# Performance work log

Hardware: AMD Instinct MI355X
Metric: run time of the kernel (lower is better)

The kernel has to match this reference:

```python
import jax, jax.numpy as jnp
import numpy as np

B, S, D, H = 4, 2048, 1024, 16
HD = D // H


def setup_inputs() -> dict:
    key = jax.random.key(0)
    ks = jax.random.split(key, 12)
    s = 1.0 / np.sqrt(D)
    return {
        "query": jax.random.normal(ks[0], (B, S, D), jnp.float32),
        "key_": jax.random.normal(ks[1], (B, S, D), jnp.float32),
        "value": jax.random.normal(ks[2], (B, S, D), jnp.float32),
        "mask": jnp.ones((1, 1, S, S), dtype=bool),
        "Wq": jax.random.normal(ks[3], (D, D), jnp.float32) * s,
        "bq": jnp.zeros((D,), jnp.float32),
        "Wk": jax.random.normal(ks[4], (D, D), jnp.float32) * s,
        "bk": jnp.zeros((D,), jnp.float32),
        "Wv": jax.random.normal(ks[5], (D, D), jnp.float32) * s,
        "bv": jnp.zeros((D,), jnp.float32),
        "Wo": jax.random.normal(ks[6], (D, D), jnp.float32) * s,
        "bo": jnp.zeros((D,), jnp.float32),
    }


def reference(query, key_, value, mask, Wq, bq, Wk, bk, Wv, bv, Wo, bo):
    # Linear projections (torch Linear: x @ W^T + b; here W stored as (in, out))
    Q = query @ Wq + bq   # [B,S,D]
    K = key_ @ Wk + bk
    V = value @ Wv + bv
    # split heads -> [B,H,S,HD]
    Q = Q.reshape(B, S, H, HD).transpose(0, 2, 1, 3)
    K = K.reshape(B, S, H, HD).transpose(0, 2, 1, 3)
    V = V.reshape(B, S, H, HD).transpose(0, 2, 1, 3)
    scores = jnp.einsum("bhqd,bhkd->bhqk", Q, K) / jnp.sqrt(jnp.float32(HD))
    scores = jnp.where(mask, scores, jnp.float32(-jnp.inf))
    attn = jax.nn.softmax(scores, axis=-1)          # [B,H,S,S]
    ctx = jnp.einsum("bhqk,bhkd->bhqd", attn, V)    # dropout = identity (eval)
    ctx = ctx.transpose(0, 2, 1, 3).reshape(B, S, D)
    out = ctx @ Wo + bo
    return out, attn
```

## Files before the change

### kernel.cpp

```cpp
#include <hip/hip_runtime.h>

typedef __attribute__((ext_vector_type(4))) unsigned short u16x4;
typedef __attribute__((ext_vector_type(8))) short short8;
typedef __attribute__((ext_vector_type(4))) short short4b;
typedef __attribute__((ext_vector_type(4))) float f32x4;

__device__ inline unsigned short f2bf(float f) {
    union { float f; unsigned int i; } v; v.f = f;
    unsigned int r = v.i + 0x7fffu + ((v.i >> 16) & 1u);
    return (unsigned short)(r >> 16);
}

#define MFMA_PV(a, b, c) __builtin_amdgcn_mfma_f32_16x16x16bf16_1k((a), (b), (c), 0, 0, 0)
#define MFMA32(a, b, c) __builtin_amdgcn_mfma_f32_16x16x32_bf16((a), (b), (c), 0, 0, 0)

#define SEXP(s) exp2f((s) * 0.18033688011112042f)

__device__ inline void gload_lds16(const unsigned short* g, unsigned short* l) {
    __builtin_amdgcn_global_load_lds(
        (const __attribute__((address_space(1))) void*)g,
        (__attribute__((address_space(3))) void*)l,
        16, 0, 0);
}

__global__ __launch_bounds__(256) void prep(const float* __restrict__ q,
                                            const float* __restrict__ k,
                                            const float* __restrict__ v,
                                            const float* __restrict__ W0,
                                            const float* __restrict__ W1,
                                            const float* __restrict__ W2,
                                            const float* __restrict__ W3,
                                            unsigned short* __restrict__ Xq,
                                            unsigned short* __restrict__ Xk,
                                            unsigned short* __restrict__ Xv,
                                            unsigned short* __restrict__ O0,
                                            unsigned short* __restrict__ O1,
                                            unsigned short* __restrict__ O2,
                                            unsigned short* __restrict__ O3) {
    __shared__ unsigned short tile[32][33];
    int bid = blockIdx.x;
    if (bid < 24576) {
        const float* in = (bid < 8192) ? q : (bid < 16384) ? k : v;
        unsigned short* out = (bid < 8192) ? Xq : (bid < 16384) ? Xk : Xv;
        int i = (bid & 8191) * 256 + threadIdx.x;
        float4 vv = ((const float4*)in)[i];
        u16x4 o = { f2bf(vv.x), f2bf(vv.y), f2bf(vv.z), f2bf(vv.w) };
        ((u16x4*)out)[i] = o;
    } else {
        int rem = bid - 24576;
        int z = rem >> 10, idx = rem & 1023;
        const float* in = (z == 0) ? W0 : (z == 1) ? W1 : (z == 2) ? W2 : W3;
        unsigned short* out = (z == 0) ? O0 : (z == 1) ? O1 : (z == 2) ? O2 : O3;
        int c0 = (idx & 31) * 32, r0 = (idx >> 5) * 32;
        int x = threadIdx.x & 31, y = threadIdx.x >> 5;
#pragma unroll
        for (int i = 0; i < 4; i++)
            tile[y + i * 8][x] = f2bf(in[(size_t)(r0 + y + i * 8) * 1024 + c0 + x]);
        __syncthreads();
#pragma unroll
        for (int i = 0; i < 4; i++)
            out[(size_t)(c0 + y + i * 8) * 1024 + r0 + x] = tile[x][y + i * 8];
    }
}

__device__ __forceinline__ void gemm_core(const unsigned short* __restrict__ X,
                                          const unsigned short* __restrict__ Wt,
                                          unsigned short* As, unsigned short* Bs,
                                          int m0, int n0, int K, f32x4 acc[4][4]) {
    const int t = threadIdx.x;
    const int l = t & 63, w = t >> 6;
    const int lg = l >> 4, ln = l & 15;
    const int wm = (w >> 1) * 64, wn = (w & 1) * 64;

    int sr[4], sc[4];
#pragma unroll
    for (int i = 0; i < 4; i++) {
        int pos = i * 2048 + t * 8;
        sr[i] = pos >> 6;
        int c8 = (pos >> 3) & 7;
        sc[i] = (c8 ^ (sr[i] & 7)) * 8;
    }

    for (int k0 = 0; k0 < K; k0 += 64) {
#pragma unroll
        for (int i = 0; i < 4; i++)
            gload_lds16(&X[(size_t)(m0 + sr[i]) * K + k0 + sc[i]], &As[i * 2048 + w * 512]);
#pragma unroll
        for (int i = 0; i < 4; i++)
            gload_lds16(&Wt[(size_t)(n0 + sr[i]) * K + k0 + sc[i]], &Bs[i * 2048 + w * 512]);
        __syncthreads();
#pragma unroll
        for (int kk = 0; kk < 2; kk++) {
            short8 af[4], bfr[4];
#pragma unroll
            for (int i = 0; i < 4; i++) {
                int sl = (((kk << 2) | lg) ^ (ln & 7)) * 8;
                af[i]  = *(const short8*)&As[(wm + i * 16 + ln) * 64 + sl];
                bfr[i] = *(const short8*)&Bs[(wn + i * 16 + ln) * 64 + sl];
            }
#pragma unroll
            for (int i = 0; i < 4; i++)
#pragma unroll
                for (int j = 0; j < 4; j++)
                    acc[i][j] = MFMA32(af[i], bfr[j], acc[i][j]);
        }
        __syncthreads();
    }
}

__global__ __launch_bounds__(256) void gemm_qk(const unsigned short* __restrict__ Xq,
                                               const unsigned short* __restrict__ Xk,
                                               const unsigned short* __restrict__ WqT,
                                               const unsigned short* __restrict__ WkT,
                                               const float* __restrict__ bq,
                                               const float* __restrict__ bk,
                                               unsigned short* __restrict__ Qp,
                                               unsigned short* __restrict__ Kt) {
    __shared__ unsigned short As[8192];
    __shared__ unsigned short Bs[8192];
    const int z = blockIdx.z;
    const unsigned short* X = z ? Xk : Xq;
    const unsigned short* Wt = z ? WkT : WqT;
    const float* bias = z ? bk : bq;
    const int t = threadIdx.x, l = t & 63, w = t >> 6;
    const int lg = l >> 4, ln = l & 15;
    const int wm = (w >> 1) * 64, wn = (w & 1) * 64;
    const int m0 = blockIdx.y * 128, n0 = blockIdx.x * 128;

    const f32x4 zero = {0.f, 0.f, 0.f, 0.f};
    f32x4 acc[4][4];
#pragma unroll
    for (int i = 0; i < 4; i++)
#pragma unroll
        for (int j = 0; j < 4; j++) acc[i][j] = zero;

    gemm_core(X, Wt, As, Bs, m0, n0, 1024, acc);

#pragma unroll
    for (int j = 0; j < 4; j++) {
        int gn = n0 + wn + j * 16 + ln;
        float bvv = bias[gn];
#pragma unroll
        for (int i = 0; i < 4; i++) {
            int gm = m0 + wm + i * 16 + 4 * lg;
#pragma unroll
            for (int jj = 0; jj < 4; jj++) {
                float val = acc[i][j][jj] + bvv;
                int m = gm + jj, n = gn;
                if (z) {
                    int b = m >> 11, s = m & 2047;
                    int itk = s >> 5, r = s & 31;
                    int h = n >> 6, dl = n & 63;
                    int cst = (dl >> 3) ^ (r & 7);
                    size_t off = (size_t)(b * 16 + h) * 131072 +
                                 (size_t)itk * 2048 + r * 64 + cst * 8 + (dl & 7);
                    Kt[off] = f2bf(val);
                } else {
                    Qp[(size_t)m * 1024 + n] = f2bf(val);
                }
            }
        }
    }
}

__global__ __launch_bounds__(256) void gemmv_pass1(const unsigned short* __restrict__ Xv,
                                                   const unsigned short* __restrict__ WvT,
                                                   const float* __restrict__ bv,
                                                   unsigned short* __restrict__ Vt,
                                                   const unsigned short* __restrict__ Qp,
                                                   const unsigned short* __restrict__ Kt,
                                                   float* __restrict__ se_buf) {
    const int S = 2048, Dm = 1024;
    __shared__ unsigned short smem[16384];

    int bid = blockIdx.x;
    int t = threadIdx.x, l = t & 63, w = t >> 6;
    int lg = l >> 4, ln = l & 15;

    if (bid >= 1024) {
        int g = bid - 1024;
        const int wm = (w >> 1) * 64, wn = (w & 1) * 64;
        const int m0 = (g >> 3) * 128, n0 = (g & 7) * 128;
        const f32x4 zero = {0.f, 0.f, 0.f, 0.f};
        f32x4 acc[4][4];
#pragma unroll
        for (int i = 0; i < 4; i++)
#pragma unroll
            for (int j = 0; j < 4; j++) acc[i][j] = zero;

        gemm_core(Xv, WvT, smem, smem + 8192, m0, n0, 1024, acc);

#pragma unroll
        for (int j = 0; j < 4; j++) {
            int gn = n0 + wn + j * 16 + ln;
            float bvv = bv[gn];
#pragma unroll
            for (int i = 0; i < 4; i++) {
                int gm = m0 + wm + i * 16 + 4 * lg;
#pragma unroll
                for (int jj = 0; jj < 4; jj++) {
                    float val = acc[i][j][jj] + bvv;
                    int m = gm + jj, n = gn;
                    int b = m >> 11, s = m & 2047;
                    int h = n >> 6, dl = n & 63;
                    size_t off = (size_t)(b * 16 + h) * 131072 +
                                 (size_t)(s >> 5) * 2048 + ((s >> 4) & 1) * 1024 +
                                 dl * 16 + (s & 15);
                    Vt[off] = f2bf(val);
                }
            }
        }
        return;
    }

    int wid = (bid & 7) * 128 + (bid >> 3);
    int qt = wid & 15, bh = wid >> 4;
    int b = bh >> 4, h = bh & 15;
    int qbase = qt * 128 + w * 16;

    const unsigned short* Qr0 = Qp + (size_t)(b * S + qbase + ln) * Dm + h * 64;
    const unsigned short* Qr1 = Qr0 + (size_t)64 * Dm;
    short8 q00 = *(const short8*)&Qr0[8 * lg];
    short8 q01 = *(const short8*)&Qr0[32 + 8 * lg];
    short8 q10 = *(const short8*)&Qr1[8 * lg];
    short8 q11 = *(const short8*)&Qr1[32 + 8 * lg];

    const unsigned short* Kb = Kt + (size_t)bh * 131072;
    const int c0x = (lg ^ (ln & 7)) * 8;
    const int c1x = ((4 + lg) ^ (ln & 7)) * 8;
    const int gb[4] = { ln * 64, 1024 + ln * 64, 2048 + ln * 64, 3072 + ln * 64 };

#define STAGE_K64(it, buf) do { \
    gload_lds16(Kb + (size_t)(it) * 4096 + t * 8, &smem[(buf) * 4096 + w * 512]); \
    gload_lds16(Kb + (size_t)(it) * 4096 + 2048 + t * 8, &smem[(buf) * 4096 + 2048 + w * 512]); } while (0)

    const f32x4 zero = {0.f, 0.f, 0.f, 0.f};
    float se0 = 0.f, se1 = 0.f;
    int cur = 0;
    STAGE_K64(0, 0);
    __syncthreads();
    for (int it = 0; it < 32; ++it) {
        if (it < 31) STAGE_K64(it + 1, cur ^ 1);
        f32x4 s0[4], s1[4];
        __builtin_amdgcn_s_setprio(1);
#pragma unroll
        for (int g = 0; g < 4; g++) {
            short8 ka = *(const short8*)&smem[cur * 4096 + gb[g] + c0x];
            short8 kb = *(const short8*)&smem[cur * 4096 + gb[g] + c1x];
            s0[g] = MFMA32(ka, q00, zero);
            s0[g] = MFMA32(kb, q01, s0[g]);
            s1[g] = MFMA32(ka, q10, zero);
            s1[g] = MFMA32(kb, q11, s1[g]);
        }
        __builtin_amdgcn_s_setprio(0);
#pragma unroll
        for (int g = 0; g < 4; g++) {
#pragma unroll
            for (int j = 0; j < 4; j++) {
                se0 += SEXP(s0[g][j]);
                se1 += SEXP(s1[g][j]);
            }
        }
        __syncthreads();
        cur ^= 1;
    }
    se0 += __shfl_xor(se0, 16); se0 += __shfl_xor(se0, 32);
    se1 += __shfl_xor(se1, 16); se1 += __shfl_xor(se1, 32);
    if (lg == 0) {
        se_buf[bh * 2048 + qbase + ln] = se0;
        se_buf[bh * 2048 + qbase + 64 + ln] = se1;
    }
#undef STAGE_K64
}

__global__ __launch_bounds__(256) void attn_pass2(const unsigned short* __restrict__ Qp,
                                                  const unsigned short* __restrict__ Kt,
                                                  const unsigned short* __restrict__ Vt,
                                                  const float* __restrict__ se_buf,
                                                  float* __restrict__ attn_out,
                                                  unsigned short* __restrict__ Ctx) {
    const int S = 2048, Dm = 1024;
    __shared__ unsigned short Ks[2][4096];
    __shared__ unsigned short Vs[2][4096];

    int blk = blockIdx.x;
    int wid = (blk & 7) * 128 + (blk >> 3);
    int qt = wid & 15, bh = wid >> 4;
    int b = bh >> 4, h = bh & 15;
    int t = threadIdx.x, l = t & 63, w = t >> 6;
    int lg = l >> 4, ln = l & 15;
    int qbase = qt * 128 + w * 16;

    const unsigned short* Qr0 = Qp + (size_t)(b * S + qbase + ln) * Dm + h * 64;
    const unsigned short* Qr1 = Qr0 + (size_t)64 * Dm;
    short8 q00 = *(const short8*)&Qr0[8 * lg];
    short8 q01 = *(const short8*)&Qr0[32 + 8 * lg];
    short8 q10 = *(const short8*)&Qr1[8 * lg];
    short8 q11 = *(const short8*)&Qr1[32 + 8 * lg];

    float inv0 = 1.0f / se_buf[bh * 2048 + qbase + ln];
    float inv1 = 1.0f / se_buf[bh * 2048 + qbase + 64 + ln];

    const unsigned short* Kb = Kt + (size_t)bh * 131072;
    const unsigned short* Vb = Vt + (size_t)bh * 131072;
    const int c0x = (lg ^ (ln & 7)) * 8;
    const int c1x = ((4 + lg) ^ (ln & 7)) * 8;
    const int gb[4] = { ln * 64, 1024 + ln * 64, 2048 + ln * 64, 3072 + ln * 64 };

#define STAGE_K64(it, buf) do { \
    gload_lds16(Kb + (size_t)(it) * 4096 + t * 8, &Ks[buf][w * 512]); \
    gload_lds16(Kb + (size_t)(it) * 4096 + 2048 + t * 8, &Ks[buf][2048 + w * 512]); } while (0)
#define STAGE_V64(it, buf) do { \
    gload_lds16(Vb + (size_t)(it) * 4096 + t * 8, &Vs[buf][w * 512]); \
    gload_lds16(Vb + (size_t)(it) * 4096 + 2048 + t * 8, &Vs[buf][2048 + w * 512]); } while (0)

    const f32x4 zero = {0.f, 0.f, 0.f, 0.f};
    f32x4 acc0[4], acc1[4];
#pragma unroll
    for (int i = 0; i < 4; i++) { acc0[i] = zero; acc1[i] = zero; }

    float* Ar0 = attn_out + ((size_t)bh * S + qbase + ln) * S;
    float* Ar1 = Ar0 + (size_t)64 * S;

    int cur = 0;
    STAGE_K64(0, 0);
    STAGE_V64(0, 0);
    __syncthreads();
    for (int it = 0; it < 32; ++it) {
        if (it < 31) { STAGE_K64(it + 1, cur ^ 1); STAGE_V64(it + 1, cur ^ 1); }
        f32x4 s0[4], s1[4];
        __builtin_amdgcn_s_setprio(1);
#pragma unroll
        for (int g = 0; g < 4; g++) {
            short8 ka = *(const short8*)&Ks[cur][gb[g] + c0x];
            short8 kb = *(const short8*)&Ks[cur][gb[g] + c1x];
            s0[g] = MFMA32(ka, q00, zero);
            s0[g] = MFMA32(kb, q01, s0[g]);
            s1[g] = MFMA32(ka, q10, zero);
            s1[g] = MFMA32(kb, q11, s1[g]);
        }
        __builtin_amdgcn_s_setprio(0);

        union { short4b v; unsigned short u[4]; } pf0[4], pf1[4];
#pragma unroll
        for (int g = 0; g < 4; g++) {
            f32x4 pw0, pw1;
#pragma unroll
            for (int j = 0; j < 4; j++) {
                float p0 = SEXP(s0[g][j]) * inv0;
                float p1 = SEXP(s1[g][j]) * inv1;
                pw0[j] = p0; pf0[g].u[j] = f2bf(p0);
                pw1[j] = p1; pf1[g].u[j] = f2bf(p1);
            }
            __builtin_nontemporal_store(pw0, (f32x4*)&Ar0[it * 64 + g * 16 + 4 * lg]);
            __builtin_nontemporal_store(pw1, (f32x4*)&Ar1[it * 64 + g * 16 + 4 * lg]);
        }

        __builtin_amdgcn_s_setprio(1);
#pragma unroll
        for (int db = 0; db < 4; db++) {
            int vbase = (db * 16 + ln) * 16 + 4 * lg;
#pragma unroll
            for (int g = 0; g < 4; g++) {
                short4b vf = *(const short4b*)&Vs[cur][g * 1024 + vbase];
                acc0[db] = MFMA_PV(pf0[g].v, vf, acc0[db]);
                acc1[db] = MFMA_PV(pf1[g].v, vf, acc1[db]);
            }
        }
        __builtin_amdgcn_s_setprio(0);
        __syncthreads();
        cur ^= 1;
    }

#pragma unroll
    for (int db = 0; db < 4; db++)
#pragma unroll
        for (int j = 0; j < 4; j++) {
            Ctx[(size_t)(b * S + qbase + 4 * lg + j) * Dm + h * 64 + db * 16 + ln] =
                f2bf(acc0[db][j]);
            Ctx[(size_t)(b * S + qbase + 64 + 4 * lg + j) * Dm + h * 64 + db * 16 + ln] =
                f2bf(acc1[db][j]);
        }
#undef STAGE_K64
#undef STAGE_V64
}

__global__ __launch_bounds__(256) void gemm_out(const unsigned short* __restrict__ X,
                                                const unsigned short* __restrict__ Wt,
                                                const float* __restrict__ bias,
                                                float* __restrict__ outp) {
    __shared__ unsigned short As[8192];
    __shared__ unsigned short Bs[8192];
    const int t = threadIdx.x, l = t & 63, w = t >> 6;
    const int lg = l >> 4, ln = l & 15;
    const int wm = (w >> 1) * 64, wn = (w & 1) * 64;
    const int m0 = blockIdx.y * 128, n0 = blockIdx.x * 128;

    const f32x4 zero = {0.f, 0.f, 0.f, 0.f};
    f32x4 acc[4][4];
#pragma unroll
    for (int i = 0; i < 4; i++)
#pragma unroll
        for (int j = 0; j < 4; j++) acc[i][j] = zero;

    gemm_core(X, Wt, As, Bs, m0, n0, 1024, acc);

#pragma unroll
    for (int j = 0; j < 4; j++) {
        int gn = n0 + wn + j * 16 + ln;
        float bvv = bias[gn];
#pragma unroll
        for (int i = 0; i < 4; i++) {
            int gm = m0 + wm + i * 16 + 4 * lg;
#pragma unroll
            for (int jj = 0; jj < 4; jj++)
                __builtin_nontemporal_store(acc[i][j][jj] + bvv,
                                            &outp[(size_t)(gm + jj) * 1024 + gn]);
        }
    }
}

extern "C" void kernel_launch(void* const* d_in, const int* in_sizes, int n_in,
                              void* d_out, int out_size, void* d_ws, size_t ws_size,
                              hipStream_t stream) {
    const float* query = (const float*)d_in[0];
    const float* key_  = (const float*)d_in[1];
    const float* value = (const float*)d_in[2];
    const float* Wq = (const float*)d_in[4];
    const float* bq = (const float*)d_in[5];
    const float* Wk = (const float*)d_in[6];
    const float* bk = (const float*)d_in[7];
    const float* Wv = (const float*)d_in[8];
    const float* bv = (const float*)d_in[9];
    const float* Wo = (const float*)d_in[10];
    const float* bo = (const float*)d_in[11];

    const size_t BSD = (size_t)4 * 2048 * 1024;
    const size_t DD  = (size_t)1024 * 1024;

    unsigned short* Xq  = (unsigned short*)d_ws;
    unsigned short* Xk  = Xq + BSD;
    unsigned short* Xv  = Xk + BSD;
    unsigned short* Qp  = Xv + BSD;
    unsigned short* Kt  = Qp + BSD;
    unsigned short* Vt  = Kt + BSD;
    unsigned short* WqT = Vt + BSD;
    unsigned short* WkT = WqT + DD;
    unsigned short* WvT = WkT + DD;
    unsigned short* WoT = WvT + DD;
    float* SE = (float*)(WoT + DD);
    unsigned short* Ctx = Xq;

    float* out0 = (float*)d_out;
    float* attn = out0 + BSD;

    dim3 tb(256);

    prep<<<dim3(28672), tb, 0, stream>>>(query, key_, value, Wq, Wk, Wv, Wo,
                                         Xq, Xk, Xv, WqT, WkT, WvT, WoT);

    gemm_qk<<<dim3(8, 64, 2), tb, 0, stream>>>(Xq, Xk, WqT, WkT, bq, bk, Qp, Kt);

    gemmv_pass1<<<dim3(1536), tb, 0, stream>>>(Xv, WvT, bv, Vt, Qp, Kt, SE);

    attn_pass2<<<dim3(1024), tb, 0, stream>>>(Qp, Kt, Vt, SE, attn, Ctx);

    gemm_out<<<dim3(8, 64), tb, 0, stream>>>(Ctx, WoT, bo, out0);
}
```

Measured before the change: 556.6 us.

## Split V GEMM from pass1, store log-sum-exp, pack bf16 conversions

```diff
diff --git a/kernel.cpp b/kernel.cpp
--- a/kernel.cpp
+++ b/kernel.cpp
@@ -1,4 +1,5 @@
 #include <hip/hip_runtime.h>
+#include <hip/hip_bf16.h>
 
 typedef __attribute__((ext_vector_type(4))) unsigned short u16x4;
 typedef __attribute__((ext_vector_type(8))) short short8;
@@ -11,10 +12,16 @@
     return (unsigned short)(r >> 16);
 }
 
+__device__ inline unsigned int pk_bf16(float a, float b) {
+    union { __hip_bfloat162 h; unsigned int u; } cv;
+    cv.h = __float22bfloat162_rn(float2{a, b});
+    return cv.u;
+}
+
 #define MFMA_PV(a, b, c) __builtin_amdgcn_mfma_f32_16x16x16bf16_1k((a), (b), (c), 0, 0, 0)
 #define MFMA32(a, b, c) __builtin_amdgcn_mfma_f32_16x16x32_bf16((a), (b), (c), 0, 0, 0)
 
-#define SEXP(s) exp2f((s) * 0.18033688011112042f)
+#define SCL 0.18033688011112042f
 
 __device__ inline void gload_lds16(const unsigned short* g, unsigned short* l) {
     __builtin_amdgcn_global_load_lds(
@@ -163,59 +170,60 @@
     }
 }
 
-__global__ __launch_bounds__(256) void gemmv_pass1(const unsigned short* __restrict__ Xv,
-                                                   const unsigned short* __restrict__ WvT,
-                                                   const float* __restrict__ bv,
-                                                   unsigned short* __restrict__ Vt,
-                                                   const unsigned short* __restrict__ Qp,
-                                                   const unsigned short* __restrict__ Kt,
-                                                   float* __restrict__ se_buf) {
+__global__ __launch_bounds__(256) void gemm_v(const unsigned short* __restrict__ Xv,
+                                              const unsigned short* __restrict__ WvT,
+                                              const float* __restrict__ bv,
+                                              unsigned short* __restrict__ Vt) {
+    __shared__ unsigned short As[8192];
+    __shared__ unsigned short Bs[8192];
+    const int t = threadIdx.x, l = t & 63, w = t >> 6;
+    const int lg = l >> 4, ln = l & 15;
+    const int wm = (w >> 1) * 64, wn = (w & 1) * 64;
+    const int m0 = blockIdx.y * 128, n0 = blockIdx.x * 128;
+
+    const f32x4 zero = {0.f, 0.f, 0.f, 0.f};
+    f32x4 acc[4][4];
+#pragma unroll
+    for (int i = 0; i < 4; i++)
+#pragma unroll
+        for (int j = 0; j < 4; j++) acc[i][j] = zero;
+
+    gemm_core(Xv, WvT, As, Bs, m0, n0, 1024, acc);
+
+#pragma unroll
+    for (int j = 0; j < 4; j++) {
+        int gn = n0 + wn + j * 16 + ln;
+        float bvv = bv[gn];
+#pragma unroll
+        for (int i = 0; i < 4; i++) {
+            int gm = m0 + wm + i * 16 + 4 * lg;
+#pragma unroll
+            for (int jj = 0; jj < 4; jj++) {
+                float val = acc[i][j][jj] + bvv;
+                int m = gm + jj, n = gn;
+                int b = m >> 11, s = m & 2047;
+                int h = n >> 6, dl = n & 63;
+                size_t off = (size_t)(b * 16 + h) * 131072 +
+                             (size_t)(s >> 5) * 2048 + ((s >> 4) & 1) * 1024 +
+                             dl * 16 + (s & 15);
+                Vt[off] = f2bf(val);
+            }
+        }
+    }
+}
+
+__global__ __launch_bounds__(256) void attn_pass1(const unsigned short* __restrict__ Qp,
+                                                  const unsigned short* __restrict__ Kt,
+                                                  float* __restrict__ lse_buf) {
     const int S = 2048, Dm = 1024;
-    __shared__ unsigned short smem[16384];
-
-    int bid = blockIdx.x;
+    __shared__ unsigned short Ks[2][4096];
+
+    int blk = blockIdx.x;
+    int wid = (blk & 7) * 128 + (blk >> 3);
+    int qt = wid & 15, bh = wid >> 4;
+    int b = bh >> 4, h = bh & 15;
     int t = threadIdx.x, l = t & 63, w = t >> 6;
     int lg = l >> 4, ln = l & 15;
-
-    if (bid >= 1024) {
-        int g = bid - 1024;
-        const int wm = (w >> 1) * 64, wn = (w & 1) * 64;
-        const int m0 = (g >> 3) * 128, n0 = (g & 7) * 128;
-        const f32x4 zero = {0.f, 0.f, 0.f, 0.f};
-        f32x4 acc[4][4];
-#pragma unroll
-        for (int i = 0; i < 4; i++)
-#pragma unroll
-            for (int j = 0; j < 4; j++) acc[i][j] = zero;
-
-        gemm_core(Xv, WvT, smem, smem + 8192, m0, n0, 1024, acc);
-
-#pragma unroll
-        for (int j = 0; j < 4; j++) {
-            int gn = n0 + wn + j * 16 + ln;
-            float bvv = bv[gn];
-#pragma unroll
-            for (int i = 0; i < 4; i++) {
-                int gm = m0 + wm + i * 16 + 4 * lg;
-#pragma unroll
-                for (int jj = 0; jj < 4; jj++) {
-                    float val = acc[i][j][jj] + bvv;
-                    int m = gm + jj, n = gn;
-                    int b = m >> 11, s = m & 2047;
-                    int h = n >> 6, dl = n & 63;
-                    size_t off = (size_t)(b * 16 + h) * 131072 +
-                                 (size_t)(s >> 5) * 2048 + ((s >> 4) & 1) * 1024 +
-                                 dl * 16 + (s & 15);
-                    Vt[off] = f2bf(val);
-                }
-            }
-        }
-        return;
-    }
-
-    int wid = (bid & 7) * 128 + (bid >> 3);
-    int qt = wid & 15, bh = wid >> 4;
-    int b = bh >> 4, h = bh & 15;
     int qbase = qt * 128 + w * 16;
 
     const unsigned short* Qr0 = Qp + (size_t)(b * S + qbase + ln) * Dm + h * 64;
@@ -231,8 +239,8 @@
     const int gb[4] = { ln * 64, 1024 + ln * 64, 2048 + ln * 64, 3072 + ln * 64 };
 
 #define STAGE_K64(it, buf) do { \
-    gload_lds16(Kb + (size_t)(it) * 4096 + t * 8, &smem[(buf) * 4096 + w * 512]); \
-    gload_lds16(Kb + (size_t)(it) * 4096 + 2048 + t * 8, &smem[(buf) * 4096 + 2048 + w * 512]); } while (0)
+    gload_lds16(Kb + (size_t)(it) * 4096 + t * 8, &Ks[buf][w * 512]); \
+    gload_lds16(Kb + (size_t)(it) * 4096 + 2048 + t * 8, &Ks[buf][2048 + w * 512]); } while (0)
 
     const f32x4 zero = {0.f, 0.f, 0.f, 0.f};
     float se0 = 0.f, se1 = 0.f;
@@ -245,8 +253,8 @@
         __builtin_amdgcn_s_setprio(1);
 #pragma unroll
         for (int g = 0; g < 4; g++) {
-            short8 ka = *(const short8*)&smem[cur * 4096 + gb[g] + c0x];
-            short8 kb = *(const short8*)&smem[cur * 4096 + gb[g] + c1x];
+            short8 ka = *(const short8*)&Ks[cur][gb[g] + c0x];
+            short8 kb = *(const short8*)&Ks[cur][gb[g] + c1x];
             s0[g] = MFMA32(ka, q00, zero);
             s0[g] = MFMA32(kb, q01, s0[g]);
             s1[g] = MFMA32(ka, q10, zero);
@@ -257,8 +265,8 @@
         for (int g = 0; g < 4; g++) {
 #pragma unroll
             for (int j = 0; j < 4; j++) {
-                se0 += SEXP(s0[g][j]);
-                se1 += SEXP(s1[g][j]);
+                se0 += exp2f(s0[g][j] * SCL);
+                se1 += exp2f(s1[g][j] * SCL);
             }
         }
         __syncthreads();
@@ -267,8 +275,8 @@
     se0 += __shfl_xor(se0, 16); se0 += __shfl_xor(se0, 32);
     se1 += __shfl_xor(se1, 16); se1 += __shfl_xor(se1, 32);
     if (lg == 0) {
-        se_buf[bh * 2048 + qbase + ln] = se0;
-        se_buf[bh * 2048 + qbase + 64 + ln] = se1;
+        lse_buf[bh * 2048 + qbase + ln] = log2f(se0);
+        lse_buf[bh * 2048 + qbase + 64 + ln] = log2f(se1);
     }
 #undef STAGE_K64
 }
@@ -276,7 +284,7 @@
 __global__ __launch_bounds__(256) void attn_pass2(const unsigned short* __restrict__ Qp,
                                                   const unsigned short* __restrict__ Kt,
                                                   const unsigned short* __restrict__ Vt,
-                                                  const float* __restrict__ se_buf,
+                                                  const float* __restrict__ lse_buf,
                                                   float* __restrict__ attn_out,
                                                   unsigned short* __restrict__ Ctx) {
     const int S = 2048, Dm = 1024;
@@ -298,8 +306,8 @@
     short8 q10 = *(const short8*)&Qr1[8 * lg];
     short8 q11 = *(const short8*)&Qr1[32 + 8 * lg];
 
-    float inv0 = 1.0f / se_buf[bh * 2048 + qbase + ln];
-    float inv1 = 1.0f / se_buf[bh * 2048 + qbase + 64 + ln];
+    float nlse0 = -lse_buf[bh * 2048 + qbase + ln];
+    float nlse1 = -lse_buf[bh * 2048 + qbase + 64 + ln];
 
     const unsigned short* Kb = Kt + (size_t)bh * 131072;
     const unsigned short* Vb = Vt + (size_t)bh * 131072;
@@ -341,17 +349,19 @@
         }
         __builtin_amdgcn_s_setprio(0);
 
-        union { short4b v; unsigned short u[4]; } pf0[4], pf1[4];
+        union { short4b v; unsigned int u2[2]; } pf0[4], pf1[4];
 #pragma unroll
         for (int g = 0; g < 4; g++) {
             f32x4 pw0, pw1;
 #pragma unroll
             for (int j = 0; j < 4; j++) {
-                float p0 = SEXP(s0[g][j]) * inv0;
-                float p1 = SEXP(s1[g][j]) * inv1;
-                pw0[j] = p0; pf0[g].u[j] = f2bf(p0);
-                pw1[j] = p1; pf1[g].u[j] = f2bf(p1);
-            }
+                pw0[j] = exp2f(fmaf(s0[g][j], SCL, nlse0));
+                pw1[j] = exp2f(fmaf(s1[g][j], SCL, nlse1));
+            }
+            pf0[g].u2[0] = pk_bf16(pw0[0], pw0[1]);
+            pf0[g].u2[1] = pk_bf16(pw0[2], pw0[3]);
+            pf1[g].u2[0] = pk_bf16(pw1[0], pw1[1]);
+            pf1[g].u2[1] = pk_bf16(pw1[2], pw1[3]);
             __builtin_nontemporal_store(pw0, (f32x4*)&Ar0[it * 64 + g * 16 + 4 * lg]);
             __builtin_nontemporal_store(pw1, (f32x4*)&Ar1[it * 64 + g * 16 + 4 * lg]);
         }
@@ -448,7 +458,7 @@
     unsigned short* WkT = WqT + DD;
     unsigned short* WvT = WkT + DD;
     unsigned short* WoT = WvT + DD;
-    float* SE = (float*)(WoT + DD);
+    float* LSE = (float*)(WoT + DD);
     unsigned short* Ctx = Xq;
 
     float* out0 = (float*)d_out;
@@ -461,9 +471,11 @@
 
     gemm_qk<<<dim3(8, 64, 2), tb, 0, stream>>>(Xq, Xk, WqT, WkT, bq, bk, Qp, Kt);
 
-    gemmv_pass1<<<dim3(1536), tb, 0, stream>>>(Xv, WvT, bv, Vt, Qp, Kt, SE);
-
-    attn_pass2<<<dim3(1024), tb, 0, stream>>>(Qp, Kt, Vt, SE, attn, Ctx);
+    attn_pass1<<<dim3(1024), tb, 0, stream>>>(Qp, Kt, LSE);
+
+    gemm_v<<<dim3(8, 64), tb, 0, stream>>>(Xv, WvT, bv, Vt);
+
+    attn_pass2<<<dim3(1024), tb, 0, stream>>>(Qp, Kt, Vt, LSE, attn, Ctx);
 
     gemm_out<<<dim3(8, 64), tb, 0, stream>>>(Ctx, WoT, bo, out0);
 }
```

Result: no change. 550.9 us (-1.0%).
